# Performance work log

Measured on AMD Instinct MI355X. Metric: run time of the kernel, lower is better.

## Reference

```python
import jax, jax.numpy as jnp
import numpy as np

B, T, F, H = 256, 128, 128, 512

def setup_inputs() -> dict:
    key = jax.random.key(0)
    ks = jax.random.split(key, 20)
    def xavier(k, shape):
        fan_in, fan_out = shape[1], shape[0]
        lim = np.sqrt(6.0 / (fan_in + fan_out)).astype(np.float32)
        return jax.random.uniform(k, shape, jnp.float32, -lim, lim)
    inp = {
        "x": jax.random.normal(ks[0], (B, T, F), jnp.float32),
        "m": (jax.random.uniform(ks[1], (B, T, F)) < 0.8).astype(jnp.float32),
        "d": jax.random.uniform(ks[2], (B, T, F), jnp.float32),
        "target_x": jax.random.normal(ks[3], (B, T, F), jnp.float32),
        "target_mask": (jax.random.uniform(ks[4], (B, T, F)) < 0.2).astype(jnp.float32),
        # TemporalDecay h: W [H,F], b [H]
        "td_h_W": xavier(ks[5], (H, F)), "td_h_b": jnp.zeros((H,), jnp.float32),
        # TemporalDecay x (diag): W [F,F], b [F]
        "td_x_W": xavier(ks[6], (F, F)), "td_x_b": jnp.zeros((F,), jnp.float32),
        # hist_reg Linear(H->F)
        "hist_W": xavier(ks[7], (F, H)), "hist_b": jnp.zeros((F,), jnp.float32),
        "feat_W": xavier(ks[8], (F, F)), "feat_b": jnp.zeros((F,), jnp.float32),
        # weight_combine Linear(2F->F)
        "wc_W": xavier(ks[9], (F, 2 * F)), "wc_b": jnp.zeros((F,), jnp.float32),
        # LSTMCell(2F -> H), PyTorch gate order i,f,g,o
        "W_ih": xavier(ks[10], (4 * H, 2 * F)), "W_hh": xavier(ks[11], (4 * H, H)),
        "b_ih": jnp.zeros((4 * H,), jnp.float32), "b_hh": jnp.zeros((4 * H,), jnp.float32),
    }
    return inp

def _rits_forward(x, m, d, target_x, target_mask,
                  td_h_W, td_h_b, td_x_W, td_x_b,
                  hist_W, hist_b, feat_W, feat_b, wc_W, wc_b,
                  W_ih, W_hh, b_ih, b_hh):
    Bx, Tx, Fx = x.shape
    Hx = td_h_W.shape[0]
    feat_mask = (1.0 - jnp.eye(Fx, dtype=x.dtype))
    feat_Wm_T = (feat_W * feat_mask).T              # [F,F]
    td_x_diag = jnp.diagonal(td_x_W)                # diag mask reduces matmul to elementwise

    def step(carry, inp):
        h, c, loss = carry
        x_t, m_t, d_t, tgt_t, ev_t = inp
        gamma_h = jnp.exp(-jax.nn.relu(d_t @ td_h_W.T + td_h_b))    # [B,H]
        gamma_x = jnp.exp(-jax.nn.relu(d_t * td_x_diag + td_x_b))   # [B,F]
        h = h * gamma_h
        x_hist = h @ hist_W.T + hist_b                              # [B,F]
        x_c = m_t * x_t + (1.0 - m_t) * x_hist
        z_h = x_c @ feat_Wm_T + feat_b
        alpha = jax.nn.sigmoid(jnp.concatenate([gamma_x, m_t], axis=1) @ wc_W.T + wc_b)
        c_h = alpha * z_h + (1.0 - alpha) * x_hist
        c_c = m_t * x_t + (1.0 - m_t) * c_h
        inputs = jnp.concatenate([c_c, m_t], axis=1)                # [B,2F]
        gates = inputs @ W_ih.T + b_ih + h @ W_hh.T + b_hh          # [B,4H]
        i_g, f_g, g_g, o_g = jnp.split(gates, 4, axis=1)
        c = jax.nn.sigmoid(f_g) * c + jax.nn.sigmoid(i_g) * jnp.tanh(g_g)
        h = jax.nn.sigmoid(o_g) * jnp.tanh(c)
        denom = ev_t.sum() + 1e-8
        loss = loss + (((x_hist - tgt_t) ** 2 * ev_t).sum()
                       + ((z_h - tgt_t) ** 2 * ev_t).sum()
                       + ((c_h - tgt_t) ** 2 * ev_t).sum()) / denom
        return (h, c, loss), c_c

    h0 = jnp.zeros((Bx, Hx), x.dtype)
    c0 = jnp.zeros((Bx, Hx), x.dtype)
    tm = lambda a: jnp.swapaxes(a, 0, 1)  # time-major [T,B,F]
    (_, _, loss), imps = jax.lax.scan(
        step, (h0, c0, jnp.float32(0.0)),
        (tm(x), tm(m), tm(d), tm(target_x), tm(target_mask)))
    imputations = jnp.swapaxes(imps, 0, 1)  # [B,T,F]
    return imputations, loss / max(Tx, 1)

def reference(x, m, d, target_x, target_mask,
              td_h_W, td_h_b, td_x_W, td_x_b,
              hist_W, hist_b, feat_W, feat_b, wc_W, wc_b,
              W_ih, W_hh, b_ih, b_hh):
    return _rits_forward(x, m, d, target_x, target_mask,
                         td_h_W, td_h_b, td_x_W, td_x_b,
                         hist_W, hist_b, feat_W, feat_b, wc_W, wc_b,
                         W_ih, W_hh, b_ih, b_hh)
```

## Files before the change

### kernel.cpp

```cpp
#include <hip/hip_runtime.h>

#define DEVINL __device__ __forceinline__

namespace {
constexpr int B = 256, T = 128, F = 128, H = 512;
constexpr int NBLK = 256;
constexpr int NTHR = 1024;

constexpr size_t OFF_NUM    = 0;
constexpr size_t OFF_DEN    = 128;
constexpr size_t OFF_WQCC   = 256;
constexpr size_t OFF_WQH    = OFF_WQCC + 64 * 2048;
constexpr size_t OFF_FSCC   = OFF_WQH + 128 * 2048;
constexpr size_t OFF_FSCHG  = OFF_FSCC + 2048;
constexpr size_t OFF_HISTQ  = OFF_FSCHG + 2048;
constexpr size_t OFF_FSCH   = OFF_HISTQ + 128 * 128;
constexpr size_t OFF_TD2    = OFF_FSCH + 128;
constexpr size_t OFF_FEAT2  = OFF_TD2 + 64 * 512;
constexpr size_t OFF_WC2    = OFF_FEAT2 + 64 * 128;
constexpr size_t OFF_BSUM   = OFF_WC2 + 128 * 128;
constexpr size_t OFF_FDIAG  = OFF_BSUM + 2048;
constexpr size_t WS_WORDS   = OFF_FDIAG + 128;

constexpr float ACT_S  = 15.875f;
constexpr float DEQ_CC = 1.f / (127.f * 15.875f);
constexpr float DEQ_H  = 1.f / (127.f * 127.f);
}

typedef _Float16 h2_t __attribute__((ext_vector_type(2)));

DEVINL h2_t as_h2(unsigned u) { union { unsigned u; h2_t h; } c; c.u = u; return c.h; }
DEVINL unsigned pack2(float a, float b) {
  union { h2_t h; unsigned u; } c;
  c.h = h2_t{(_Float16)a, (_Float16)b};
  return c.u;
}

#if defined(__has_builtin)
#if __has_builtin(__builtin_amdgcn_fdot2)
#define HAVE_FDOT2 1
#endif
#if __has_builtin(__builtin_amdgcn_sdot4)
#define HAVE_SDOT4 1
#endif
#endif
#ifdef HAVE_FDOT2
DEVINL float fdot2(h2_t a, h2_t b, float c) { return __builtin_amdgcn_fdot2(a, b, c, false); }
#else
DEVINL float fdot2(h2_t a, h2_t b, float c) {
  return fmaf((float)a.x, (float)b.x, fmaf((float)a.y, (float)b.y, c));
}
#endif
#ifdef HAVE_SDOT4
DEVINL int sdot4(int a, int b, int c) { return __builtin_amdgcn_sdot4(a, b, c, false); }
#else
DEVINL int sdot4(int a, int b, int c) {
  return c + ((a << 24) >> 24) * ((b << 24) >> 24)
           + ((a << 16) >> 24) * ((b << 16) >> 24)
           + ((a << 8) >> 24) * ((b << 8) >> 24)
           + (a >> 24) * (b >> 24);
}
#endif

DEVINL float fast_sig(float x)  { return 1.f / (1.f + __expf(-x)); }
DEVINL float fast_tanh(float x) { return 1.f - 2.f / (1.f + __expf(2.f * x)); }

DEVINL float wave_sum(float v) {
#pragma unroll
  for (int s = 32; s; s >>= 1) v += __shfl_down(v, s, 64);
  return v;
}
DEVINL float wave_max(float v) {
#pragma unroll
  for (int s = 32; s; s >>= 1) v = fmaxf(v, __shfl_down(v, s, 64));
  return v;
}

__global__ void prep_f16(const float* __restrict__ td_h_W, const float* __restrict__ feat_W,
                         const float* __restrict__ wc_W, const float* __restrict__ b_ih,
                         const float* __restrict__ b_hh,
                         unsigned* __restrict__ wsu, float* __restrict__ wsf) {
  int idx = blockIdx.x * blockDim.x + threadIdx.x;
  if (idx < 32768) {
    const int k2 = idx >> 9, j = idx & 511;
    wsu[OFF_TD2 + idx] = pack2(td_h_W[j * 128 + 2 * k2], td_h_W[j * 128 + 2 * k2 + 1]);
  } else if (idx < 40960) {
    const int i = idx - 32768, k2 = i >> 7, f = i & 127;
    wsu[OFF_FEAT2 + i] = pack2(feat_W[f * 128 + 2 * k2], feat_W[f * 128 + 2 * k2 + 1]);
  } else if (idx < 57344) {
    const int i = idx - 40960, k2 = i >> 7, f = i & 127;
    wsu[OFF_WC2 + i] = pack2(wc_W[f * 256 + 2 * k2], wc_W[f * 256 + 2 * k2 + 1]);
  } else if (idx < 59392) {
    const int i = idx - 57344, unit = i >> 2, g = i & 3;
    wsf[OFF_BSUM + i] = b_ih[g * 512 + unit] + b_hh[g * 512 + unit];
  } else if (idx < 59520) {
    const int f = idx - 59392;
    wsf[OFF_FDIAG + f] = (float)(_Float16)feat_W[f * 129];
  }
}

__global__ void prep_quant_wih(const float* __restrict__ Wih,
                               unsigned* __restrict__ wq, float* __restrict__ fscc) {
  const int col = blockIdx.x;
  const int unit = col >> 2, g = col & 3;
  const float* src = Wih + (size_t)(g * 512 + unit) * 256;
  const int t = threadIdx.x;
  const float4 v = ((const float4*)src)[t];
  float mx = fmaxf(fmaxf(fabsf(v.x), fabsf(v.y)), fmaxf(fabsf(v.z), fabsf(v.w)));
  mx = wave_max(mx);
  mx = __shfl(mx, 0, 64);
  const float s = (mx > 0.f) ? 127.f / mx : 0.f;
  const int q0 = __float2int_rn(v.x * s), q1 = __float2int_rn(v.y * s);
  const int q2 = __float2int_rn(v.z * s), q3 = __float2int_rn(v.w * s);
  wq[t * 2048 + col] =
      (q0 & 0xFF) | ((q1 & 0xFF) << 8) | ((q2 & 0xFF) << 16) | ((q3 & 0xFF) << 24);
  if (t == 0) fscc[col] = mx * DEQ_CC;
}

__global__ void prep_quant_whh(const float* __restrict__ Whh,
                               unsigned* __restrict__ wq, float* __restrict__ fschg) {
  const int col = blockIdx.x;
  const int unit = col >> 2, g = col & 3;
  const float* src = Whh + (size_t)(g * 512 + unit) * 512;
  const int t = threadIdx.x;
  const float4 v = ((const float4*)src)[t];
  float mx = fmaxf(fmaxf(fabsf(v.x), fabsf(v.y)), fmaxf(fabsf(v.z), fabsf(v.w)));
  mx = wave_max(mx);
  __shared__ float wm[2];
  if ((t & 63) == 0) wm[t >> 6] = mx;
  __syncthreads();
  const float maxv = fmaxf(wm[0], wm[1]);
  const float s = (maxv > 0.f) ? 127.f / maxv : 0.f;
  const int q0 = __float2int_rn(v.x * s), q1 = __float2int_rn(v.y * s);
  const int q2 = __float2int_rn(v.z * s), q3 = __float2int_rn(v.w * s);
  wq[t * 2048 + col] =
      (q0 & 0xFF) | ((q1 & 0xFF) << 8) | ((q2 & 0xFF) << 16) | ((q3 & 0xFF) << 24);
  if (t == 0) fschg[col] = maxv * DEQ_H;
}

__global__ void prep_quant_hist(const float* __restrict__ histW,
                                unsigned* __restrict__ histq, float* __restrict__ fsch) {
  const int f = blockIdx.x;
  const float* src = histW + (size_t)f * 512;
  const int t = threadIdx.x;
  const float4 v = ((const float4*)src)[t];
  float mx = fmaxf(fmaxf(fabsf(v.x), fabsf(v.y)), fmaxf(fabsf(v.z), fabsf(v.w)));
  mx = wave_max(mx);
  __shared__ float wm[2];
  if ((t & 63) == 0) wm[t >> 6] = mx;
  __syncthreads();
  const float maxv = fmaxf(wm[0], wm[1]);
  const float s = (maxv > 0.f) ? 127.f / maxv : 0.f;
  const int q0 = __float2int_rn(v.x * s), q1 = __float2int_rn(v.y * s);
  const int q2 = __float2int_rn(v.z * s), q3 = __float2int_rn(v.w * s);
  histq[t * 128 + f] =
      (q0 & 0xFF) | ((q1 & 0xFF) << 8) | ((q2 & 0xFF) << 16) | ((q3 & 0xFF) << 24);
  if (t == 0) fsch[f] = maxv * DEQ_H;
}

__global__ void __launch_bounds__(1024) rits_batch(
    const float* __restrict__ x, const float* __restrict__ m, const float* __restrict__ d,
    const float* __restrict__ tx, const float* __restrict__ tmask,
    const float* __restrict__ td_h_b, const float* __restrict__ td_x_W,
    const float* __restrict__ td_x_b, const float* __restrict__ hist_b,
    const float* __restrict__ feat_b, const float* __restrict__ wc_b,
    const unsigned* __restrict__ wsu, const float* __restrict__ wsf,
    float* __restrict__ num, float* __restrict__ den, float* __restrict__ out)
{
  const int tid = threadIdx.x;
  const int row = blockIdx.x;
  const int unit = tid & 511;
  const int kh = tid >> 9;

  __shared__ unsigned actq[64];
  __shared__ int hq[128];
  __shared__ unsigned d2[64];
  __shared__ unsigned xc2[64];
  __shared__ unsigned gxm2[128];
  __shared__ float xrow[128], mrow[128], drow[128], txrow[128], evrow[128];
  __shared__ int   partI[1024];
  __shared__ float partZ[1024], partA[1024];
  __shared__ int4  partHc[512], partHh[512];
  __shared__ float redA[2], redB[2];

  const float4 bs    = *(const float4*)(wsf + OFF_BSUM + 4 * unit);
  const float4 fscc4 = *(const float4*)(wsf + OFF_FSCC + 4 * unit);
  const float4 fsch4 = *(const float4*)(wsf + OFF_FSCHG + 4 * unit);
  const float tdb = td_h_b[unit];
  const int fc = tid & 127;
  const float hb = hist_b[fc], fb = feat_b[fc], wb = wc_b[fc];
  const float fd = wsf[OFF_FDIAG + fc];
  const float dxw = td_x_W[fc * 129], dxb = td_x_b[fc];
  const float fsch_f = wsf[OFF_FSCH + fc];

  float h0 = 0.f, c0 = 0.f;

  for (int t = 0; t < T; ++t) {
    const int base = (row * T + t) * F;
    float xh_r = 0.f, xc_r = 0.f;

    if (tid < 640) {
      const int a = tid >> 7, f = tid & 127;
      const float v = (a == 0 ? x[base + f] : a == 1 ? m[base + f] : a == 2 ? d[base + f]
                       : a == 3 ? tx[base + f] : tmask[base + f]);
      if      (a == 0) xrow[f]  = v;
      else if (a == 1) mrow[f]  = v;
      else if (a == 2) drow[f]  = v;
      else if (a == 3) txrow[f] = v;
      else             evrow[f] = v;
    } else if (tid < 704) {
      const int k2 = tid - 640;
      d2[k2] = pack2(d[base + 2 * k2], d[base + 2 * k2 + 1]);
    } else if (tid < 768) {
      const int q = tid - 704;
      gxm2[64 + q] = pack2(m[base + 2 * q], m[base + 2 * q + 1]);
    } else if (tid < 800) {
      const int w = tid - 768;
      const int b4 = base + 4 * w;
      const int q0 = __float2int_rn(m[b4] * ACT_S);
      const int q1 = __float2int_rn(m[b4 + 1] * ACT_S);
      const int q2 = __float2int_rn(m[b4 + 2] * ACT_S);
      const int q3 = __float2int_rn(m[b4 + 3] * ACT_S);
      actq[32 + w] =
          (q0 & 0xFF) | ((q1 & 0xFF) << 8) | ((q2 & 0xFF) << 16) | ((q3 & 0xFF) << 24);
    }
    __syncthreads();

    if (tid < 512) {
      float g0 = tdb;
#pragma unroll 8
      for (int k2 = 0; k2 < 64; ++k2)
        g0 = fdot2(as_h2(wsu[OFF_TD2 + (k2 << 9) + tid]), as_h2(d2[k2]), g0);
      h0 *= __expf(-fmaxf(g0, 0.f));
      int q = __float2int_rn(h0 * 127.f);
      const int a1 = __shfl_down(q, 1, 64), a2 = __shfl_down(q, 2, 64), a3 = __shfl_down(q, 3, 64);
      if ((tid & 3) == 0)
        hq[tid >> 2] =
            (q & 0xFF) | ((a1 & 0xFF) << 8) | ((a2 & 0xFF) << 16) | ((a3 & 0xFF) << 24);
    }
    __syncthreads();

    {
      const int kq = tid >> 7;
      int isum = 0;
#pragma unroll 8
      for (int k = 0; k < 16; ++k) {
        const int k4 = kq * 16 + k;
        isum = sdot4((int)wsu[OFF_HISTQ + (k4 << 7) + fc], hq[k4], isum);
      }
      partI[tid] = isum;
    }
    __syncthreads();

    if (tid < 128) {
      int isum = 0;
#pragma unroll
      for (int i = 0; i < 8; ++i) isum += partI[tid + 128 * i];
      xh_r = fmaf((float)isum, fsch_f, hb);
      const float gx = __expf(-fmaxf(fmaf(drow[tid], dxw, dxb), 0.f));
      const float mv = mrow[tid];
      xc_r = mv * xrow[tid] + (1.f - mv) * xh_r;
      const float xcs = __shfl_down(xc_r, 1, 64);
      const float gxs = __shfl_down(gx, 1, 64);
      if (!(tid & 1)) {
        xc2[tid >> 1]  = pack2(xc_r, xcs);
        gxm2[tid >> 1] = pack2(gx, gxs);
      }
    }
    __syncthreads();

    {
      const int kq = tid >> 7;
      float zs = 0.f;
#pragma unroll 8
      for (int k = 0; k < 8; ++k) {
        const int k2 = kq * 8 + k;
        zs = fdot2(as_h2(wsu[OFF_FEAT2 + (k2 << 7) + fc]), as_h2(xc2[k2]), zs);
      }
      partZ[tid] = zs;
      float as = 0.f;
#pragma unroll 8
      for (int k = 0; k < 16; ++k) {
        const int k2 = kq * 16 + k;
        as = fdot2(as_h2(wsu[OFF_WC2 + (k2 << 7) + fc]), as_h2(gxm2[k2]), as);
      }
      partA[tid] = as;
    }
    __syncthreads();

    if (tid < 128) {
      float z = fb, aa = wb;
#pragma unroll
      for (int i = 0; i < 8; ++i) { z += partZ[tid + 128 * i]; aa += partA[tid + 128 * i]; }
      z -= xc_r * fd;
      const float al = fast_sig(aa);
      const float ch = al * z + (1.f - al) * xh_r;
      const float mv = mrow[tid];
      const float cc = mv * xrow[tid] + (1.f - mv) * ch;
      out[base + tid] = cc;
      const float ev = evrow[tid], tg = txrow[tid];
      const float e1 = xh_r - tg, e2 = z - tg, e3 = ch - tg;
      const float s1 = wave_sum(ev * (e1 * e1 + e2 * e2 + e3 * e3));
      const float s2 = wave_sum(ev);
      if ((tid & 63) == 0) { redA[tid >> 6] = s1; redB[tid >> 6] = s2; }
      int qc = __float2int_rn(fminf(fmaxf(cc, -8.f), 8.f) * ACT_S);
      const int c1s = __shfl_down(qc, 1, 64), c2s = __shfl_down(qc, 2, 64), c3s = __shfl_down(qc, 3, 64);
      if (!(tid & 3))
        actq[tid >> 2] =
            (qc & 0xFF) | ((c1s & 0xFF) << 8) | ((c2s & 0xFF) << 16) | ((c3s & 0xFF) << 24);
    }
    __syncthreads();

    {
      if (tid == 1023) {
        atomicAdd(&num[t], redA[0] + redA[1]);
        atomicAdd(&den[t], redB[0] + redB[1]);
      }
      int ci = 0, cf = 0, cg = 0, co = 0;
      const unsigned* wq = wsu + OFF_WQCC + 4 * unit;
#pragma unroll 8
      for (int k = 0; k < 32; ++k) {
        const int k4 = kh * 32 + k;
        const uint4 w = *(const uint4*)(wq + (k4 << 11));
        const int a0 = (int)actq[k4];
        ci = sdot4((int)w.x, a0, ci); cf = sdot4((int)w.y, a0, cf);
        cg = sdot4((int)w.z, a0, cg); co = sdot4((int)w.w, a0, co);
      }
      int hi = 0, hf = 0, hg = 0, ho = 0;
      const unsigned* wh = wsu + OFF_WQH + 4 * unit;
#pragma unroll 8
      for (int k = 0; k < 64; ++k) {
        const int k4 = kh * 64 + k;
        const uint4 w = *(const uint4*)(wh + (k4 << 11));
        const int a0 = hq[k4];
        hi = sdot4((int)w.x, a0, hi); hf = sdot4((int)w.y, a0, hf);
        hg = sdot4((int)w.z, a0, hg); ho = sdot4((int)w.w, a0, ho);
      }
      if (tid >= 512) {
        partHc[unit] = int4{ci, cf, cg, co};
        partHh[unit] = int4{hi, hf, hg, ho};
      }
      __syncthreads();
      if (tid < 512) {
        const int4 pc = partHc[unit], ph = partHh[unit];
        const float ai = bs.x + fscc4.x * (float)(ci + pc.x) + fsch4.x * (float)(hi + ph.x);
        const float af = bs.y + fscc4.y * (float)(cf + pc.y) + fsch4.y * (float)(hf + ph.y);
        const float ag = bs.z + fscc4.z * (float)(cg + pc.z) + fsch4.z * (float)(hg + ph.z);
        const float ao = bs.w + fscc4.w * (float)(co + pc.w) + fsch4.w * (float)(ho + ph.w);
        const float ig = fast_sig(ai), fg = fast_sig(af);
        const float gg = fast_tanh(ag), og = fast_sig(ao);
        c0 = fg * c0 + ig * gg;
        h0 = og * fast_tanh(c0);
      }
    }
    __syncthreads();
  }
}

__global__ void finalize(const float* __restrict__ num, const float* __restrict__ den,
                         float* __restrict__ out) {
  __shared__ float red[2];
  const int t = threadIdx.x;
  float v = num[t] / (den[t] + 1e-8f);
  v = wave_sum(v);
  if ((t & 63) == 0) red[t >> 6] = v;
  __syncthreads();
  if (t == 0) out[(size_t)B * T * F] = (red[0] + red[1]) / (float)T;
}

extern "C" void kernel_launch(void* const* d_in, const int* in_sizes, int n_in,
                              void* d_out, int out_size, void* d_ws, size_t ws_size,
                              hipStream_t stream) {
  const float* x      = (const float*)d_in[0];
  const float* m      = (const float*)d_in[1];
  const float* d      = (const float*)d_in[2];
  const float* tx     = (const float*)d_in[3];
  const float* tmask  = (const float*)d_in[4];
  const float* td_h_W = (const float*)d_in[5];
  const float* td_h_b = (const float*)d_in[6];
  const float* td_x_W = (const float*)d_in[7];
  const float* td_x_b = (const float*)d_in[8];
  const float* hist_W = (const float*)d_in[9];
  const float* hist_b = (const float*)d_in[10];
  const float* feat_W = (const float*)d_in[11];
  const float* feat_b = (const float*)d_in[12];
  const float* wc_W   = (const float*)d_in[13];
  const float* wc_b   = (const float*)d_in[14];
  const float* W_ih   = (const float*)d_in[15];
  const float* W_hh   = (const float*)d_in[16];
  const float* b_ih   = (const float*)d_in[17];
  const float* b_hh   = (const float*)d_in[18];

  float*    wsf = (float*)d_ws;
  unsigned* wsu = (unsigned*)d_ws;
  float*    out = (float*)d_out;

  if (ws_size < WS_WORDS * 4) return;

  hipMemsetAsync(d_ws, 0, 256 * sizeof(float), stream);
  prep_f16<<<dim3((59520 + 255) / 256), dim3(256), 0, stream>>>(
      td_h_W, feat_W, wc_W, b_ih, b_hh, wsu, wsf);
  prep_quant_wih<<<dim3(2048), dim3(64), 0, stream>>>(
      W_ih, wsu + OFF_WQCC, wsf + OFF_FSCC);
  prep_quant_whh<<<dim3(2048), dim3(128), 0, stream>>>(
      W_hh, wsu + OFF_WQH, wsf + OFF_FSCHG);
  prep_quant_hist<<<dim3(128), dim3(128), 0, stream>>>(
      hist_W, wsu + OFF_HISTQ, wsf + OFF_FSCH);
  rits_batch<<<dim3(NBLK), dim3(NTHR), 0, stream>>>(
      x, m, d, tx, tmask, td_h_b, td_x_W, td_x_b, hist_b, feat_b, wc_b,
      wsu, wsf, wsf + OFF_NUM, wsf + OFF_DEN, out);
  finalize<<<dim3(1), dim3(128), 0, stream>>>(wsf + OFF_NUM, wsf + OFF_DEN, out);
}
```

Baseline: 2.436 ms.

## Overlap feature chain in one wave with h-recurrent LSTM matvec

The per-step feature path (history regression, feature regression, weight combine, loss and output) is moved into a single wavefront, each lane handling two features over full K with vectorized uint4 weight loads. Meanwhile the other 960 threads compute the W_hh·h gate partials concurrently, since those depend only on the decayed h. Weights are transposed to row-major-per-output in prep so that loads are contiguous, gamma_x is computed during the input load phase, and several block barriers are removed. The cost is a long serial chain on one wave, which may become the critical path, and less parallelism for the feature matvecs.

New measurement: 4.241 ms. +74.1%, slower.

```diff
diff --git a/kernel.cpp b/kernel.cpp
--- a/kernel.cpp
+++ b/kernel.cpp
@@ -82,13 +82,13 @@
                          unsigned* __restrict__ wsu, float* __restrict__ wsf) {
   int idx = blockIdx.x * blockDim.x + threadIdx.x;
   if (idx < 32768) {
-    const int k2 = idx >> 9, j = idx & 511;
-    wsu[OFF_TD2 + idx] = pack2(td_h_W[j * 128 + 2 * k2], td_h_W[j * 128 + 2 * k2 + 1]);
+    const int u = idx >> 6, k2 = idx & 63;
+    wsu[OFF_TD2 + idx] = pack2(td_h_W[u * 128 + 2 * k2], td_h_W[u * 128 + 2 * k2 + 1]);
   } else if (idx < 40960) {
-    const int i = idx - 32768, k2 = i >> 7, f = i & 127;
+    const int i = idx - 32768, f = i >> 6, k2 = i & 63;
     wsu[OFF_FEAT2 + i] = pack2(feat_W[f * 128 + 2 * k2], feat_W[f * 128 + 2 * k2 + 1]);
   } else if (idx < 57344) {
-    const int i = idx - 40960, k2 = i >> 7, f = i & 127;
+    const int i = idx - 40960, f = i >> 7, k2 = i & 127;
     wsu[OFF_WC2 + i] = pack2(wc_W[f * 256 + 2 * k2], wc_W[f * 256 + 2 * k2 + 1]);
   } else if (idx < 59392) {
     const int i = idx - 57344, unit = i >> 2, g = i & 3;
@@ -153,12 +153,12 @@
   const float s = (maxv > 0.f) ? 127.f / maxv : 0.f;
   const int q0 = __float2int_rn(v.x * s), q1 = __float2int_rn(v.y * s);
   const int q2 = __float2int_rn(v.z * s), q3 = __float2int_rn(v.w * s);
-  histq[t * 128 + f] =
+  histq[f * 128 + t] =
       (q0 & 0xFF) | ((q1 & 0xFF) << 8) | ((q2 & 0xFF) << 16) | ((q3 & 0xFF) << 24);
   if (t == 0) fsch[f] = maxv * DEQ_H;
 }
 
-__global__ void __launch_bounds__(1024) rits_batch(
+__global__ void __launch_bounds__(NTHR) rits_batch(
     const float* __restrict__ x, const float* __restrict__ m, const float* __restrict__ d,
     const float* __restrict__ tx, const float* __restrict__ tmask,
     const float* __restrict__ td_h_b, const float* __restrict__ td_x_W,
@@ -169,191 +169,209 @@
 {
   const int tid = threadIdx.x;
   const int row = blockIdx.x;
+  const int lane = tid & 63, wv = tid >> 6;
+
+  __shared__ __align__(16) unsigned actq_s[64];
+  __shared__ __align__(16) int      hq_s[128];
+  __shared__ __align__(16) unsigned d2_s[64];
+  __shared__ __align__(16) unsigned xc2_s[64];
+  __shared__ __align__(16) unsigned gxm2_s[128];
+  __shared__ float x_s[128], m_s[128], tx_s[128], ev_s[128];
+  __shared__ float dxw_s[128], dxb_s[128];
+  __shared__ int4  partHh_s[1024];
+  __shared__ int4  partHc_s[512];
+
   const int unit = tid & 511;
-  const int kh = tid >> 9;
-
-  __shared__ unsigned actq[64];
-  __shared__ int hq[128];
-  __shared__ unsigned d2[64];
-  __shared__ unsigned xc2[64];
-  __shared__ unsigned gxm2[128];
-  __shared__ float xrow[128], mrow[128], drow[128], txrow[128], evrow[128];
-  __shared__ int   partI[1024];
-  __shared__ float partZ[1024], partA[1024];
-  __shared__ int4  partHc[512], partHh[512];
-  __shared__ float redA[2], redB[2];
-
   const float4 bs    = *(const float4*)(wsf + OFF_BSUM + 4 * unit);
   const float4 fscc4 = *(const float4*)(wsf + OFF_FSCC + 4 * unit);
   const float4 fsch4 = *(const float4*)(wsf + OFF_FSCHG + 4 * unit);
   const float tdb = td_h_b[unit];
-  const int fc = tid & 127;
-  const float hb = hist_b[fc], fb = feat_b[fc], wb = wc_b[fc];
-  const float fd = wsf[OFF_FDIAG + fc];
-  const float dxw = td_x_W[fc * 129], dxb = td_x_b[fc];
-  const float fsch_f = wsf[OFF_FSCH + fc];
+
+  float2 fsf2{}, hb2{}, fb2{}, wb2{}, fd2{};
+  if (tid < 64) {
+    fsf2 = *(const float2*)(wsf + OFF_FSCH + 2 * tid);
+    hb2  = *(const float2*)(hist_b + 2 * tid);
+    fb2  = *(const float2*)(feat_b + 2 * tid);
+    wb2  = *(const float2*)(wc_b + 2 * tid);
+    fd2  = *(const float2*)(wsf + OFF_FDIAG + 2 * tid);
+  }
+  if (tid < 128) { dxw_s[tid] = td_x_W[tid * 129]; dxb_s[tid] = td_x_b[tid]; }
 
   float h0 = 0.f, c0 = 0.f;
+  __syncthreads();
 
   for (int t = 0; t < T; ++t) {
     const int base = (row * T + t) * F;
-    float xh_r = 0.f, xc_r = 0.f;
-
-    if (tid < 640) {
+
+    if (tid < 512) {
       const int a = tid >> 7, f = tid & 127;
-      const float v = (a == 0 ? x[base + f] : a == 1 ? m[base + f] : a == 2 ? d[base + f]
-                       : a == 3 ? tx[base + f] : tmask[base + f]);
-      if      (a == 0) xrow[f]  = v;
-      else if (a == 1) mrow[f]  = v;
-      else if (a == 2) drow[f]  = v;
-      else if (a == 3) txrow[f] = v;
-      else             evrow[f] = v;
+      const float v = (a == 0 ? x[base + f] : a == 1 ? m[base + f]
+                       : a == 2 ? tx[base + f] : tmask[base + f]);
+      if      (a == 0) x_s[f]  = v;
+      else if (a == 1) m_s[f]  = v;
+      else if (a == 2) tx_s[f] = v;
+      else             ev_s[f] = v;
+    } else if (tid < 576) {
+      const int j = tid - 512;
+      d2_s[j] = pack2(d[base + 2 * j], d[base + 2 * j + 1]);
+    } else if (tid < 640) {
+      const int j = tid - 576;
+      gxm2_s[64 + j] = pack2(m[base + 2 * j], m[base + 2 * j + 1]);
     } else if (tid < 704) {
-      const int k2 = tid - 640;
-      d2[k2] = pack2(d[base + 2 * k2], d[base + 2 * k2 + 1]);
-    } else if (tid < 768) {
-      const int q = tid - 704;
-      gxm2[64 + q] = pack2(m[base + 2 * q], m[base + 2 * q + 1]);
-    } else if (tid < 800) {
-      const int w = tid - 768;
+      const int j = tid - 640;
+      const float dv0 = d[base + 2 * j], dv1 = d[base + 2 * j + 1];
+      const float gx0 = __expf(-fmaxf(fmaf(dv0, dxw_s[2 * j], dxb_s[2 * j]), 0.f));
+      const float gx1 = __expf(-fmaxf(fmaf(dv1, dxw_s[2 * j + 1], dxb_s[2 * j + 1]), 0.f));
+      gxm2_s[j] = pack2(gx0, gx1);
+    } else if (tid < 736) {
+      const int w = tid - 704;
       const int b4 = base + 4 * w;
       const int q0 = __float2int_rn(m[b4] * ACT_S);
       const int q1 = __float2int_rn(m[b4 + 1] * ACT_S);
       const int q2 = __float2int_rn(m[b4 + 2] * ACT_S);
       const int q3 = __float2int_rn(m[b4 + 3] * ACT_S);
-      actq[32 + w] =
+      actq_s[32 + w] =
           (q0 & 0xFF) | ((q1 & 0xFF) << 8) | ((q2 & 0xFF) << 16) | ((q3 & 0xFF) << 24);
     }
     __syncthreads();
 
     if (tid < 512) {
       float g0 = tdb;
+      const uint4* tw = (const uint4*)(wsu + OFF_TD2 + (size_t)tid * 64);
+      const uint4* dw = (const uint4*)d2_s;
 #pragma unroll 8
-      for (int k2 = 0; k2 < 64; ++k2)
-        g0 = fdot2(as_h2(wsu[OFF_TD2 + (k2 << 9) + tid]), as_h2(d2[k2]), g0);
+      for (int q = 0; q < 16; ++q) {
+        const uint4 w = tw[q], dd = dw[q];
+        g0 = fdot2(as_h2(w.x), as_h2(dd.x), g0);
+        g0 = fdot2(as_h2(w.y), as_h2(dd.y), g0);
+        g0 = fdot2(as_h2(w.z), as_h2(dd.z), g0);
+        g0 = fdot2(as_h2(w.w), as_h2(dd.w), g0);
+      }
       h0 *= __expf(-fmaxf(g0, 0.f));
       int q = __float2int_rn(h0 * 127.f);
       const int a1 = __shfl_down(q, 1, 64), a2 = __shfl_down(q, 2, 64), a3 = __shfl_down(q, 3, 64);
       if ((tid & 3) == 0)
-        hq[tid >> 2] =
+        hq_s[tid >> 2] =
             (q & 0xFF) | ((a1 & 0xFF) << 8) | ((a2 & 0xFF) << 16) | ((a3 & 0xFF) << 24);
     }
     __syncthreads();
 
-    {
-      const int kq = tid >> 7;
-      int isum = 0;
+    if (wv == 0) {
+      const int L = tid;
+      int is0 = 0, is1 = 0;
+      {
+        const uint4* hq4 = (const uint4*)hq_s;
+        const uint4* hw0 = (const uint4*)(wsu + OFF_HISTQ + (size_t)(2 * L) * 128);
+        const uint4* hw1 = (const uint4*)(wsu + OFF_HISTQ + (size_t)(2 * L + 1) * 128);
 #pragma unroll 8
-      for (int k = 0; k < 16; ++k) {
-        const int k4 = kq * 16 + k;
-        isum = sdot4((int)wsu[OFF_HISTQ + (k4 << 7) + fc], hq[k4], isum);
-      }
-      partI[tid] = isum;
+        for (int k = 0; k < 32; ++k) {
+          const uint4 a = hq4[k];
+          const uint4 w0 = hw0[k], w1 = hw1[k];
+          is0 = sdot4((int)w0.x, (int)a.x, is0); is1 = sdot4((int)w1.x, (int)a.x, is1);
+          is0 = sdot4((int)w0.y, (int)a.y, is0); is1 = sdot4((int)w1.y, (int)a.y, is1);
+          is0 = sdot4((int)w0.z, (int)a.z, is0); is1 = sdot4((int)w1.z, (int)a.z, is1);
+          is0 = sdot4((int)w0.w, (int)a.w, is0); is1 = sdot4((int)w1.w, (int)a.w, is1);
+        }
+      }
+      const float xh0 = fmaf((float)is0, fsf2.x, hb2.x);
+      const float xh1 = fmaf((float)is1, fsf2.y, hb2.y);
+      const float mv0 = m_s[2 * L], mv1 = m_s[2 * L + 1];
+      const float xv0 = x_s[2 * L], xv1 = x_s[2 * L + 1];
+      const float xc0 = mv0 * xv0 + (1.f - mv0) * xh0;
+      const float xc1 = mv1 * xv1 + (1.f - mv1) * xh1;
+      xc2_s[L] = pack2(xc0, xc1);
+      float z0 = fb2.x, z1 = fb2.y, aa0 = wb2.x, aa1 = wb2.y;
+      {
+        const uint4* fw0 = (const uint4*)(wsu + OFF_FEAT2 + (size_t)(2 * L) * 64);
+        const uint4* fw1 = (const uint4*)(wsu + OFF_FEAT2 + (size_t)(2 * L + 1) * 64);
+        const uint4* xcw = (const uint4*)xc2_s;
+#pragma unroll 8
+        for (int k = 0; k < 16; ++k) {
+          const uint4 w0 = fw0[k], w1 = fw1[k], xv = xcw[k];
+          z0 = fdot2(as_h2(w0.x), as_h2(xv.x), z0); z1 = fdot2(as_h2(w1.x), as_h2(xv.x), z1);
+          z0 = fdot2(as_h2(w0.y), as_h2(xv.y), z0); z1 = fdot2(as_h2(w1.y), as_h2(xv.y), z1);
+          z0 = fdot2(as_h2(w0.z), as_h2(xv.z), z0); z1 = fdot2(as_h2(w1.z), as_h2(xv.z), z1);
+          z0 = fdot2(as_h2(w0.w), as_h2(xv.w), z0); z1 = fdot2(as_h2(w1.w), as_h2(xv.w), z1);
+        }
+        const uint4* ww0 = (const uint4*)(wsu + OFF_WC2 + (size_t)(2 * L) * 128);
+        const uint4* ww1 = (const uint4*)(wsu + OFF_WC2 + (size_t)(2 * L + 1) * 128);
+        const uint4* gw = (const uint4*)gxm2_s;
+#pragma unroll 8
+        for (int k = 0; k < 32; ++k) {
+          const uint4 w0 = ww0[k], w1 = ww1[k], gv = gw[k];
+          aa0 = fdot2(as_h2(w0.x), as_h2(gv.x), aa0); aa1 = fdot2(as_h2(w1.x), as_h2(gv.x), aa1);
+          aa0 = fdot2(as_h2(w0.y), as_h2(gv.y), aa0); aa1 = fdot2(as_h2(w1.y), as_h2(gv.y), aa1);
+          aa0 = fdot2(as_h2(w0.z), as_h2(gv.z), aa0); aa1 = fdot2(as_h2(w1.z), as_h2(gv.z), aa1);
+          aa0 = fdot2(as_h2(w0.w), as_h2(gv.w), aa0); aa1 = fdot2(as_h2(w1.w), as_h2(gv.w), aa1);
+        }
+      }
+      z0 -= xc0 * fd2.x; z1 -= xc1 * fd2.y;
+      const float al0 = fast_sig(aa0), al1 = fast_sig(aa1);
+      const float ch0 = al0 * z0 + (1.f - al0) * xh0;
+      const float ch1 = al1 * z1 + (1.f - al1) * xh1;
+      const float cc0 = mv0 * xv0 + (1.f - mv0) * ch0;
+      const float cc1 = mv1 * xv1 + (1.f - mv1) * ch1;
+      ((float2*)(out + base))[L] = float2{cc0, cc1};
+      const float tg0 = tx_s[2 * L], tg1 = tx_s[2 * L + 1];
+      const float ev0 = ev_s[2 * L], ev1 = ev_s[2 * L + 1];
+      const float e10 = xh0 - tg0, e20 = z0 - tg0, e30 = ch0 - tg0;
+      const float e11 = xh1 - tg1, e21 = z1 - tg1, e31 = ch1 - tg1;
+      float s1 = ev0 * (e10 * e10 + e20 * e20 + e30 * e30)
+               + ev1 * (e11 * e11 + e21 * e21 + e31 * e31);
+      float s2 = ev0 + ev1;
+      s1 = wave_sum(s1); s2 = wave_sum(s2);
+      if (L == 0) { atomicAdd(&num[t], s1); atomicAdd(&den[t], s2); }
+      const int q0 = __float2int_rn(fminf(fmaxf(cc0, -8.f), 8.f) * ACT_S);
+      const int q1 = __float2int_rn(fminf(fmaxf(cc1, -8.f), 8.f) * ACT_S);
+      const unsigned u16 = (unsigned)(q0 & 0xFF) | ((unsigned)(q1 & 0xFF) << 8);
+      const unsigned o16 = __shfl_down(u16, 1, 64);
+      if (!(L & 1)) actq_s[L >> 1] = u16 | (o16 << 16);
+    } else {
+      const int t1 = tid - 64;
+      for (int tt = t1; tt < 1024; tt += 960) {
+        const int u2 = tt & 511, khh = tt >> 9;
+        const unsigned* wp = wsu + OFF_WQH + ((size_t)khh * 64) * 2048 + 4 * u2;
+        const int* hqp = hq_s + khh * 64;
+        int hi = 0, hf = 0, hg = 0, ho = 0;
+#pragma unroll 16
+        for (int k = 0; k < 64; ++k) {
+          const uint4 w = *(const uint4*)(wp + (size_t)k * 2048);
+          const int a0 = hqp[k];
+          hi = sdot4((int)w.x, a0, hi); hf = sdot4((int)w.y, a0, hf);
+          hg = sdot4((int)w.z, a0, hg); ho = sdot4((int)w.w, a0, ho);
+        }
+        partHh_s[tt] = int4{hi, hf, hg, ho};
+      }
     }
     __syncthreads();
 
-    if (tid < 128) {
-      int isum = 0;
-#pragma unroll
-      for (int i = 0; i < 8; ++i) isum += partI[tid + 128 * i];
-      xh_r = fmaf((float)isum, fsch_f, hb);
-      const float gx = __expf(-fmaxf(fmaf(drow[tid], dxw, dxb), 0.f));
-      const float mv = mrow[tid];
-      xc_r = mv * xrow[tid] + (1.f - mv) * xh_r;
-      const float xcs = __shfl_down(xc_r, 1, 64);
-      const float gxs = __shfl_down(gx, 1, 64);
-      if (!(tid & 1)) {
-        xc2[tid >> 1]  = pack2(xc_r, xcs);
-        gxm2[tid >> 1] = pack2(gx, gxs);
-      }
-    }
-    __syncthreads();
-
     {
-      const int kq = tid >> 7;
-      float zs = 0.f;
-#pragma unroll 8
-      for (int k = 0; k < 8; ++k) {
-        const int k2 = kq * 8 + k;
-        zs = fdot2(as_h2(wsu[OFF_FEAT2 + (k2 << 7) + fc]), as_h2(xc2[k2]), zs);
-      }
-      partZ[tid] = zs;
-      float as = 0.f;
-#pragma unroll 8
-      for (int k = 0; k < 16; ++k) {
-        const int k2 = kq * 16 + k;
-        as = fdot2(as_h2(wsu[OFF_WC2 + (k2 << 7) + fc]), as_h2(gxm2[k2]), as);
-      }
-      partA[tid] = as;
-    }
-    __syncthreads();
-
-    if (tid < 128) {
-      float z = fb, aa = wb;
-#pragma unroll
-      for (int i = 0; i < 8; ++i) { z += partZ[tid + 128 * i]; aa += partA[tid + 128 * i]; }
-      z -= xc_r * fd;
-      const float al = fast_sig(aa);
-      const float ch = al * z + (1.f - al) * xh_r;
-      const float mv = mrow[tid];
-      const float cc = mv * xrow[tid] + (1.f - mv) * ch;
-      out[base + tid] = cc;
-      const float ev = evrow[tid], tg = txrow[tid];
-      const float e1 = xh_r - tg, e2 = z - tg, e3 = ch - tg;
-      const float s1 = wave_sum(ev * (e1 * e1 + e2 * e2 + e3 * e3));
-      const float s2 = wave_sum(ev);
-      if ((tid & 63) == 0) { redA[tid >> 6] = s1; redB[tid >> 6] = s2; }
-      int qc = __float2int_rn(fminf(fmaxf(cc, -8.f), 8.f) * ACT_S);
-      const int c1s = __shfl_down(qc, 1, 64), c2s = __shfl_down(qc, 2, 64), c3s = __shfl_down(qc, 3, 64);
-      if (!(tid & 3))
-        actq[tid >> 2] =
-            (qc & 0xFF) | ((c1s & 0xFF) << 8) | ((c2s & 0xFF) << 16) | ((c3s & 0xFF) << 24);
-    }
-    __syncthreads();
-
-    {
-      if (tid == 1023) {
-        atomicAdd(&num[t], redA[0] + redA[1]);
-        atomicAdd(&den[t], redB[0] + redB[1]);
-      }
+      const int kh = tid >> 9;
       int ci = 0, cf = 0, cg = 0, co = 0;
       const unsigned* wq = wsu + OFF_WQCC + 4 * unit;
-#pragma unroll 8
+#pragma unroll 16
       for (int k = 0; k < 32; ++k) {
         const int k4 = kh * 32 + k;
-        const uint4 w = *(const uint4*)(wq + (k4 << 11));
-        const int a0 = (int)actq[k4];
+        const uint4 w = *(const uint4*)(wq + ((size_t)k4 << 11));
+        const int a0 = (int)actq_s[k4];
         ci = sdot4((int)w.x, a0, ci); cf = sdot4((int)w.y, a0, cf);
         cg = sdot4((int)w.z, a0, cg); co = sdot4((int)w.w, a0, co);
       }
-      int hi = 0, hf = 0, hg = 0, ho = 0;
-      const unsigned* wh = wsu + OFF_WQH + 4 * unit;
-#pragma unroll 8
-      for (int k = 0; k < 64; ++k) {
-        const int k4 = kh * 64 + k;
-        const uint4 w = *(const uint4*)(wh + (k4 << 11));
-        const int a0 = hq[k4];
-        hi = sdot4((int)w.x, a0, hi); hf = sdot4((int)w.y, a0, hf);
-        hg = sdot4((int)w.z, a0, hg); ho = sdot4((int)w.w, a0, ho);
-      }
-      if (tid >= 512) {
-        partHc[unit] = int4{ci, cf, cg, co};
-        partHh[unit] = int4{hi, hf, hg, ho};
-      }
+      if (tid >= 512) partHc_s[unit] = int4{ci, cf, cg, co};
       __syncthreads();
       if (tid < 512) {
-        const int4 pc = partHc[unit], ph = partHh[unit];
-        const float ai = bs.x + fscc4.x * (float)(ci + pc.x) + fsch4.x * (float)(hi + ph.x);
-        const float af = bs.y + fscc4.y * (float)(cf + pc.y) + fsch4.y * (float)(hf + ph.y);
-        const float ag = bs.z + fscc4.z * (float)(cg + pc.z) + fsch4.z * (float)(hg + ph.z);
-        const float ao = bs.w + fscc4.w * (float)(co + pc.w) + fsch4.w * (float)(ho + ph.w);
+        const int4 pc = partHc_s[unit];
+        const int4 p0 = partHh_s[unit], p1 = partHh_s[unit + 512];
+        const float ai = bs.x + fscc4.x * (float)(ci + pc.x) + fsch4.x * (float)(p0.x + p1.x);
+        const float af = bs.y + fscc4.y * (float)(cf + pc.y) + fsch4.y * (float)(p0.y + p1.y);
+        const float ag = bs.z + fscc4.z * (float)(cg + pc.z) + fsch4.z * (float)(p0.z + p1.z);
+        const float ao = bs.w + fscc4.w * (float)(co + pc.w) + fsch4.w * (float)(p0.w + p1.w);
         const float ig = fast_sig(ai), fg = fast_sig(af);
         const float gg = fast_tanh(ag), og = fast_sig(ao);
         c0 = fg * c0 + ig * gg;
         h0 = og * fast_tanh(c0);
       }
     }
-    __syncthreads();
   }
 }
 
```
